# Optimization experiments

Hardware: AMD Instinct MI355X
Metric: run time of the kernel (lower is better)

Reference implementation:

```python
import jax, jax.numpy as jnp
import numpy as np

B, T, HID = 2, 2048, 1024
NH = 8
QK_DIM = 1024
V_DIM = 2048
SCALE_BASE = 512.0
GN_EPS = 1e-5


def _xpos_rotate(x, downscale):
    # x: [B, T, QK_DIM]; XPOS rotary embedding (syncdoth/RetNet, offset=0)
    d = QK_DIM
    dh = d // 2
    pos = jnp.arange(T, dtype=jnp.float32)
    # per-pair magnitude scale
    base_scale = (jnp.arange(0, d, 2, dtype=jnp.float32) + 0.4 * d) / (1.4 * d)  # [dh]
    scale = base_scale[None, :] ** (pos[:, None] / SCALE_BASE)  # [T, dh]
    if downscale:
        scale = 1.0 / scale
    inv_freq = 1.0 / (10000.0 ** (jnp.arange(dh, dtype=jnp.float32) / dh))
    sinusoid = pos[:, None] * inv_freq[None, :]  # [T, dh]
    sin = jnp.sin(sinusoid) * scale
    cos = jnp.cos(sinusoid) * scale
    # duplicate_interleave -> [T, d]
    sin = jnp.repeat(sin, 2, axis=-1)
    cos = jnp.repeat(cos, 2, axis=-1)
    x1 = x[..., 0::2]
    x2 = x[..., 1::2]
    rot = jnp.stack((-x2, x1), axis=-1).reshape(x.shape)  # rotate_every_two
    return x * cos[None] + rot * sin[None]


def setup_inputs() -> dict:
    key = jax.random.key(0)
    k1, k2, k3, k4 = jax.random.split(key, 4)
    x = jax.random.normal(k1, (B, T, HID), dtype=jnp.float32)
    Wqkv = jax.random.normal(k2, (HID, 2 * QK_DIM + V_DIM), dtype=jnp.float32) / np.sqrt(HID)
    Wg = jax.random.normal(k3, (HID, V_DIM), dtype=jnp.float32) / np.sqrt(HID)
    Wp = jax.random.normal(k4, (V_DIM, HID), dtype=jnp.float32) / np.sqrt(V_DIM)
    bp = jnp.zeros((HID,), dtype=jnp.float32)
    return {"x": x, "Wqkv": Wqkv, "Wg": Wg, "Wp": Wp, "bp": bp}


def reference(x, Wqkv, Wg, Wp, bp):
    # multi-scale decay (non-default gamma path)
    gamma = 1.0 - jnp.exp(jnp.linspace(np.log(1.0 / 32), np.log(1.0 / 512), NH)).astype(jnp.float32)  # [NH]

    qkv = x @ Wqkv  # [B,T,2qk+v]
    q, k, v = jnp.split(qkv, [QK_DIM, 2 * QK_DIM], axis=-1)
    q = _xpos_rotate(q, downscale=False)
    k = _xpos_rotate(k, downscale=True)

    dqk = QK_DIM // NH
    dv = V_DIM // NH
    q = q.reshape(B, T, NH, dqk).transpose(0, 2, 1, 3)  # [B,H,T,dqk]
    k = k.reshape(B, T, NH, dqk).transpose(0, 2, 1, 3)
    v = v.reshape(B, T, NH, dv).transpose(0, 2, 1, 3)   # [B,H,T,dv]

    # parallel decay mask: gamma^(i-j) for i>=j else 0  -> [H,T,T]
    idx = jnp.arange(T)
    expo = idx[:, None] - idx[None, :]
    expo_safe = jnp.where(expo >= 0, expo, 0).astype(jnp.float32)
    decay_mask = jnp.where(expo[None] >= 0, gamma[:, None, None] ** expo_safe[None], 0.0)  # [H,T,T]

    scores = jnp.einsum('bhid,bhjd->bhij', q, k) * (dqk ** -0.5)
    retention = jnp.einsum('bhij,bhjv->bhiv', scores * decay_mask[None], v)  # [B,H,T,dv]

    # current_kv state: sum_t decay_mask[h,-1,t] * k_t (outer) v_t  -> [B,H,dqk,dv]
    curr_kv = jnp.einsum('bhtk,bhtv,ht->bhkv', k, v, decay_mask[:, -1, :])

    ret = retention.transpose(0, 2, 1, 3).reshape(B, T, V_DIM)

    # GroupNorm(num_groups=NH, affine=False) over [B*T, V_DIM]
    g = ret.reshape(B, T, NH, dv)
    mu = jnp.mean(g, axis=-1, keepdims=True)
    var = jnp.var(g, axis=-1, keepdims=True)
    normed = ((g - mu) / jnp.sqrt(var + GN_EPS)).reshape(B, T, V_DIM)

    gate = jax.nn.silu(x @ Wg)
    out = (gate * normed) @ Wp + bp
    return out, curr_kv
```

## Files before the change

kernel.cpp:

```cpp
#include <hip/hip_runtime.h>

typedef unsigned short u16;
typedef unsigned int   u32;
typedef unsigned long long u64;

typedef __attribute__((ext_vector_type(8))) short bf8_t;
typedef __attribute__((ext_vector_type(4))) float f4_t;

#define DEVI __device__ __forceinline__
#define MFMA16(a,b,c) __builtin_amdgcn_mfma_f32_16x16x32_bf16((a),(b),(c),0,0,0)

#define BB   2
#define TT   2048
#define HIDN 1024
#define L0f  (-3.4657359027997265f)
#define DLf  (-0.3960841031714215f)
#define SCL  (0.08838834764831845f)

DEVI u16 f2b(float f) {
    u32 u = __float_as_uint(f);
    u += 0x7FFFu + ((u >> 16) & 1u);
    return (u16)(u >> 16);
}
DEVI float b2f(u16 u) { return __uint_as_float(((u32)u) << 16); }

DEVI void gll16(const void* g, void* l) {
    __builtin_amdgcn_global_load_lds((const __attribute__((address_space(1))) void*)g,
                                     (__attribute__((address_space(3))) void*)l, 16, 0, 0);
}

__global__ __launch_bounds__(256) void k_tables(u32* __restrict__ cqp, u32* __restrict__ ckp,
                                                float* __restrict__ gt, float* __restrict__ gk) {
    int bx = blockIdx.x;
    if (bx >= 4096) {
        int i = (bx - 4096) * 256 + threadIdx.x;
        if (i < 16384) {
            int h = i >> 11, t = i & 2047;
            float lg2 = log2f(1.f - expf(L0f + (float)h * DLf));
            gt[i] = exp2f((float)(2047 - t) * lg2);
        } else {
            int idx = i - 16384;
            int h = idx >> 6, d = idx & 63;
            float lg2 = log2f(1.f - expf(L0f + (float)h * DLf));
            gk[idx] = exp2f(-(float)d * lg2);
        }
        return;
    }
    int idx = bx * 256 + threadIdx.x;
    int t = idx >> 9, m = idx & 511;
    float base = (2.f * (float)m + 409.6f) * (1.f / 1433.6f);
    float s = exp2f(log2f(base) * ((float)t * (1.f / 512.f)));
    float invf = exp2f(-(float)m * (13.287712379549449f / 512.f));
    float sn, cs;
    sincosf((float)t * invf, &sn, &cs);
    int h = m >> 6;
    float lg2h = log2f(1.f - expf(L0f + (float)h * DLf));
    float qf = s * SCL * exp2f((float)(t & 63) * lg2h);
    cqp[idx] = (u32)f2b(cs * qf) | ((u32)f2b(sn * qf) << 16);
    float is = 1.f / s;
    ckp[idx] = (u32)f2b(cs * is) | ((u32)f2b(sn * is) << 16);
}

__global__ __launch_bounds__(256) void k_cvt(const float* __restrict__ in, u16* __restrict__ out) {
    int i = blockIdx.x * 256 + threadIdx.x;
    float4 v = ((const float4*)in)[i];
    u64 pk = (u64)f2b(v.x) | ((u64)f2b(v.y) << 16) | ((u64)f2b(v.z) << 32) | ((u64)f2b(v.w) << 48);
    ((u64*)out)[i] = pk;
}

__global__ __launch_bounds__(256) void k_tposeF(const float* __restrict__ Wqkv,
                                                const float* __restrict__ Wg,
                                                const float* __restrict__ Wp,
                                                u16* __restrict__ oQ, u16* __restrict__ oG,
                                                u16* __restrict__ oP) {
    __shared__ float tile[32][33];
    int bx = blockIdx.x;
    const float* in; u16* out; int R, C, cx, ry;
    if (bx < 4096)      { in = Wqkv; out = oQ; R = 1024; C = 4096; cx = bx & 127;        ry = bx >> 7; }
    else if (bx < 6144) { int b2 = bx - 4096; in = Wg; out = oG; R = 1024; C = 2048; cx = b2 & 63; ry = b2 >> 6; }
    else                { int b2 = bx - 6144; in = Wp; out = oP; R = 2048; C = 1024; cx = b2 & 31; ry = b2 >> 5; }
    int c0 = cx * 32, r0 = ry * 32;
    int tx = threadIdx.x, ty = threadIdx.y;
#pragma unroll
    for (int i = 0; i < 4; i++)
        tile[ty * 4 + i][tx] = in[(size_t)(r0 + ty * 4 + i) * C + c0 + tx];
    __syncthreads();
#pragma unroll
    for (int i = 0; i < 4; i++)
        out[(size_t)(c0 + ty * 4 + i) * R + r0 + tx] = f2b(tile[tx][ty * 4 + i]);
}

DEVI void stage_chunk(const u16* __restrict__ A, const u16* __restrict__ B,
                      int m0, int n0, int kt, char* buf, int id, int wid, int lane) {
    int j = id & 3;
    int flat = j * 8192 + wid * 1024 + lane * 16;
    int row = flat >> 7, byt = (flat & 127) ^ ((row & 7) << 4);
    if (id < 4)
        gll16((const char*)A + (size_t)(m0 + row) * 2048 + kt * 128 + byt,
              buf + j * 8192 + wid * 1024);
    else
        gll16((const char*)B + (size_t)(n0 + row) * 2048 + kt * 128 + byt,
              buf + 32768 + j * 8192 + wid * 1024);
}

#define QCORE(kk, fmh, LOADB)                                                         \
    {                                                                                 \
        bf8_t a_[4];                                                                  \
        _Pragma("unroll")                                                             \
        for (int f = 0; f < 4; f++) {                                                 \
            int ra = 128 * wr + ((fmh) * 4 + f) * 16 + lr;                            \
            a_[f] = *(const bf8_t*)(bA + ra * 128 + (((kk) * 64 + lg * 16) ^ ((ra & 7) << 4))); \
        }                                                                             \
        if (LOADB) {                                                                  \
            _Pragma("unroll")                                                         \
            for (int f = 0; f < 4; f++) {                                             \
                int rb = 64 * wc + f * 16 + lr;                                       \
                breg[f] = *(const bf8_t*)(bB + rb * 128 + (((kk) * 64 + lg * 16) ^ ((rb & 7) << 4))); \
            }                                                                         \
        }                                                                             \
        __builtin_amdgcn_s_barrier();                                                 \
        __builtin_amdgcn_s_setprio(1);                                                \
        _Pragma("unroll")                                                             \
        for (int f = 0; f < 4; f++)                                                   \
            _Pragma("unroll")                                                         \
            for (int j = 0; j < 4; j++)                                               \
                acc[(fmh) * 4 + f][j] = MFMA16(a_[f], breg[j], acc[(fmh) * 4 + f][j]); \
        __builtin_amdgcn_s_setprio(0);                                                \
    }

__global__ __launch_bounds__(512, 2) void k_gemm_qkvg8(
    const u16* __restrict__ xb, const u16* __restrict__ Wcat,
    const u32* __restrict__ cqp, const u32* __restrict__ ckp, const float* __restrict__ gkt,
    u16* __restrict__ qw, u16* __restrict__ kw, u16* __restrict__ kT, u16* __restrict__ vT,
    u16* __restrict__ gateb) {
    __shared__ __align__(16) char L[131072];
    int flat = blockIdx.x;
    int swz = (flat & 7) * 48 + (flat >> 3);
    int m0 = (swz / 24) * 256, n0 = (swz % 24) * 256;
    int tid = threadIdx.x, lane = tid & 63, wid = tid >> 6;
    int wr = wid >> 2, wc = wid & 3, lr = lane & 15, lg = lane >> 4;
    f4_t acc[8][4];
#pragma unroll
    for (int i = 0; i < 8; i++)
#pragma unroll
        for (int j = 0; j < 4; j++)
#pragma unroll
            for (int e = 0; e < 4; e++) acc[i][j][e] = 0.f;
    stage_chunk(xb, Wcat, m0, n0, 0, L, 0, wid, lane);
    stage_chunk(xb, Wcat, m0, n0, 0, L, 2, wid, lane);
    stage_chunk(xb, Wcat, m0, n0, 0, L, 4, wid, lane);
    stage_chunk(xb, Wcat, m0, n0, 0, L, 5, wid, lane);
    stage_chunk(xb, Wcat, m0, n0, 0, L, 6, wid, lane);
    stage_chunk(xb, Wcat, m0, n0, 0, L, 7, wid, lane);
    stage_chunk(xb, Wcat, m0, n0, 0, L, 1, wid, lane);
    stage_chunk(xb, Wcat, m0, n0, 0, L, 3, wid, lane);
    asm volatile("s_waitcnt vmcnt(2)" ::: "memory");
    __builtin_amdgcn_s_barrier();
    for (int kt = 0; kt < 16; ++kt) {
        const char* bA = L + (kt & 1) * 65536;
        const char* bB = bA + 32768;
        char* nbuf = L + ((kt + 1) & 1) * 65536;
        bf8_t breg[4];
        if (kt < 15) {
            stage_chunk(xb, Wcat, m0, n0, kt + 1, nbuf, 0, wid, lane);
            stage_chunk(xb, Wcat, m0, n0, kt + 1, nbuf, 2, wid, lane);
        }
        QCORE(0, 0, 1)
        if (kt < 15) { asm volatile("s_waitcnt vmcnt(2)" ::: "memory"); }
        else         { asm volatile("s_waitcnt vmcnt(0)" ::: "memory"); }
        __builtin_amdgcn_s_barrier();
        if (kt < 15) {
            stage_chunk(xb, Wcat, m0, n0, kt + 1, nbuf, 4, wid, lane);
            stage_chunk(xb, Wcat, m0, n0, kt + 1, nbuf, 5, wid, lane);
        }
        QCORE(0, 1, 0)
        __builtin_amdgcn_s_barrier();
        if (kt < 15) {
            stage_chunk(xb, Wcat, m0, n0, kt + 1, nbuf, 6, wid, lane);
            stage_chunk(xb, Wcat, m0, n0, kt + 1, nbuf, 7, wid, lane);
        }
        QCORE(1, 0, 1)
        __builtin_amdgcn_s_barrier();
        if (kt < 15) {
            stage_chunk(xb, Wcat, m0, n0, kt + 1, nbuf, 1, wid, lane);
            stage_chunk(xb, Wcat, m0, n0, kt + 1, nbuf, 3, wid, lane);
        }
        QCORE(1, 1, 0)
        if (kt < 15) { asm volatile("s_waitcnt vmcnt(2)" ::: "memory"); }
        __builtin_amdgcn_s_barrier();
    }
    __syncthreads();
    char* SP = L;
    int b = m0 >> 11, t0 = m0 & 2047;
    if (n0 < 4096 && n0 >= 2048) {
        int h = (n0 - 2048) >> 8;
#pragma unroll
        for (int fm = 0; fm < 8; fm++)
#pragma unroll
            for (int fn = 0; fn < 4; fn++) {
                int dv = wc * 64 + fn * 16 + lr;
                int rowb = wr * 128 + fm * 16 + lg * 4;
                u64 pk = 0;
#pragma unroll
                for (int r = 0; r < 4; r++) pk |= ((u64)f2b(acc[fm][fn][r])) << (16 * r);
                *(u64*)(SP + dv * 512 + ((rowb * 2) ^ ((dv & 15) << 4))) = pk;
            }
        __syncthreads();
#pragma unroll
        for (int it = 0; it < 16; it++) {
            int chunk = it * 512 + tid;
            int dv = chunk >> 5, j = chunk & 31;
            uint4 v = *(const uint4*)(SP + dv * 512 + ((j * 16) ^ ((dv & 15) << 4)));
            *(uint4*)(vT + ((size_t)((b * 8 + h) * 256 + dv)) * 2048 + t0 + j * 8) = v;
        }
    } else if (n0 < 2048) {
        int isK = n0 >= 1024;
        const u32* cT = isK ? ckp : cqp;
        int hb = (n0 >> 7) & 7;
#pragma unroll
        for (int fm = 0; fm < 8; fm++)
#pragma unroll
            for (int fn = 0; fn < 4; fn++) {
                int col = wc * 64 + fn * 16 + lr;
                int gq = (n0 & 1023) + col;
                int mi = gq >> 1, h = gq >> 7;
                u64 pk = 0;
#pragma unroll
                for (int r = 0; r < 4; r++) {
                    int rowl = wr * 128 + fm * 16 + lg * 4 + r;
                    int t = t0 + rowl;
                    float v = acc[fm][fn][r];
                    float pv = __shfl_xor(v, 1);
                    u32 cp = cT[t * 512 + mi];
                    float cs = b2f((u16)cp), sn = b2f((u16)(cp >> 16));
                    float o = (col & 1) ? (v * cs + pv * sn) : (v * cs - pv * sn);
                    if (isK) {
                        pk |= ((u64)f2b(o)) << (16 * r);
                        o *= gkt[h * 64 + (t & 63)];
                    }
                    *(u16*)(SP + rowl * 512 + ((col * 2) ^ ((rowl & 15) << 4))) = f2b(o);
                }
                if (isK)
                    *(u64*)&kT[((size_t)((b * 8 + h) * 128 + (gq & 127))) * 2048 + t0 + wr * 128 + fm * 16 + lg * 4] = pk;
            }
        __syncthreads();
#pragma unroll
        for (int it = 0; it < 16; it++) {
            int chunk = it * 512 + tid;
            int r = chunk >> 5, j = chunk & 31;
            uint4 v = *(const uint4*)(SP + r * 512 + ((j * 16) ^ ((r & 15) << 4)));
            int hh = hb + (j >> 4);
            u16* g = (isK ? kw : qw) + ((size_t)((b * 8 + hh) * 2048 + t0 + r)) * 128 + (j & 15) * 8;
            *(uint4*)g = v;
        }
    } else {
        int c0 = n0 - 4096;
#pragma unroll
        for (int fm = 0; fm < 8; fm++)
#pragma unroll
            for (int fn = 0; fn < 4; fn++) {
                int col = wc * 64 + fn * 16 + lr;
#pragma unroll
                for (int r = 0; r < 4; r++) {
                    int rowl = wr * 128 + fm * 16 + lg * 4 + r;
                    float gg = acc[fm][fn][r];
                    *(u16*)(SP + rowl * 512 + ((col * 2) ^ ((rowl & 15) << 4))) = f2b(gg / (1.f + expf(-gg)));
                }
            }
        __syncthreads();
#pragma unroll
        for (int it = 0; it < 16; it++) {
            int chunk = it * 512 + tid;
            int r = chunk >> 5, j = chunk & 31;
            uint4 v = *(const uint4*)(SP + r * 512 + ((j * 16) ^ ((r & 15) << 4)));
            *(uint4*)(gateb + (size_t)(b * 2048 + t0 + r) * 2048 + c0 + j * 8) = v;
        }
    }
}

DEVI void gemm_ml(const u16* __restrict__ Ag, const u16* __restrict__ Bg, int Klen, int Kstr,
                  int m0, int n0, u16* As, u16* Bs, f4_t acc[4][4]) {
    int tid = threadIdx.x, lane = tid & 63, wid = tid >> 6;
    int wr = wid >> 1, wc = wid & 1, lr = lane & 15, lg = lane >> 4;
    for (int k0 = 0; k0 < Klen; k0 += 64) {
        __syncthreads();
#pragma unroll
        for (int p = 0; p < 4; p++) {
            int flat = p * 4096 + tid * 16;
            int row = flat >> 7, byt = (flat & 127) ^ ((row & 7) << 4);
            gll16((const char*)Ag + ((size_t)(m0 + row) * Kstr + k0) * 2 + byt,
                  (char*)As + p * 4096 + wid * 1024);
            gll16((const char*)Bg + ((size_t)(n0 + row) * Kstr + k0) * 2 + byt,
                  (char*)Bs + p * 4096 + wid * 1024);
        }
        __syncthreads();
#pragma unroll
        for (int kk = 0; kk < 2; kk++) {
            bf8_t a[4], b[4];
#pragma unroll
            for (int f = 0; f < 4; f++) {
                int ra = wr * 64 + f * 16 + lr;
                a[f] = *(const bf8_t*)((const char*)As + ra * 128 + ((kk * 64 + lg * 16) ^ ((ra & 7) << 4)));
                int rb = wc * 64 + f * 16 + lr;
                b[f] = *(const bf8_t*)((const char*)Bs + rb * 128 + ((kk * 64 + lg * 16) ^ ((rb & 7) << 4)));
            }
#pragma unroll
            for (int i = 0; i < 4; i++)
#pragma unroll
                for (int j = 0; j < 4; j++)
                    acc[i][j] = MFMA16(a[i], b[j], acc[i][j]);
        }
    }
}

DEVI void acc_zero(f4_t acc[4][4]) {
#pragma unroll
    for (int i = 0; i < 4; i++)
#pragma unroll
        for (int j = 0; j < 4; j++)
#pragma unroll
            for (int e = 0; e < 4; e++) acc[i][j][e] = 0.f;
}

__global__ __launch_bounds__(256) void k_gemm_outp(const u16* __restrict__ gdb, const u16* __restrict__ Wt,
                                                   float* __restrict__ part) {
    __shared__ u16 SM[128 * 128];
    f4_t acc[4][4]; acc_zero(acc);
    int m0 = blockIdx.y * 128, n0 = blockIdx.x * 128, kz = blockIdx.z;
    gemm_ml(gdb + kz * 1024, Wt + kz * 1024, 1024, 2048, m0, n0, SM, SM + 128 * 64, acc);
    int tid = threadIdx.x, lane = tid & 63, wid = tid >> 6;
    int wr = wid >> 1, wc = wid & 1, lr = lane & 15, lg = lane >> 4;
    float* SMf = (float*)SM;
    float* po = part + (size_t)kz * 4096 * 1024;
    __syncthreads();
#pragma unroll
    for (int p = 0; p < 2; p++) {
        if (p) __syncthreads();
        if (wr == p) {
#pragma unroll
            for (int fm = 0; fm < 4; fm++)
#pragma unroll
                for (int fn = 0; fn < 4; fn++) {
                    int col = wc * 64 + fn * 16 + lr;
#pragma unroll
                    for (int r = 0; r < 4; r++) {
                        int rowl = fm * 16 + lg * 4 + r;
                        *(float*)((char*)SMf + rowl * 512 + ((col * 4) ^ ((rowl & 7) << 6))) = acc[fm][fn][r];
                    }
                }
        }
        __syncthreads();
#pragma unroll
        for (int it2 = 0; it2 < 8; it2++) {
            int chunk = it2 * 256 + tid;
            int rowl = chunk >> 5, j = chunk & 31;
            f4_t v = *(const f4_t*)((const char*)SMf + rowl * 512 + ((j * 16) ^ ((rowl & 7) << 6)));
            *(f4_t*)((char*)po + ((size_t)(m0 + p * 64 + rowl) * 1024 + n0) * 4 + j * 16) = v;
        }
    }
}

__global__ __launch_bounds__(256) void k_outred(const float* __restrict__ part, const float* __restrict__ bp,
                                                float* __restrict__ outp) {
    int i = blockIdx.x * 256 + threadIdx.x;
    f4_t a = ((const f4_t*)part)[i];
    f4_t c = ((const f4_t*)(part + (size_t)4096 * 1024))[i];
    f4_t bb = *(const f4_t*)(bp + ((i * 4) & 1023));
#pragma unroll
    for (int e = 0; e < 4; e++) a[e] += c[e] + bb[e];
    ((f4_t*)outp)[i] = a;
}

__global__ __launch_bounds__(256, 3) void k_retention(const u16* __restrict__ qws, const u16* __restrict__ kws,
                                                      const u16* __restrict__ vTws,
                                                      u16* __restrict__ ret0, u16* __restrict__ ret1) {
    __shared__ u16 SMr[64 * 128 + 256 * 64];
    u16* Ks = SMr;
    u16* Vs = SMr + 64 * 128;
    int x = blockIdx.x;
    int it, jlo, jhi, toret1;
    if (x < 16)      { it = 15 - x;  jlo = 0;              jhi = it + 1;         toret1 = 0; }
    else if (x < 32) { it = x;       jlo = 0;              jhi = (it + 2) >> 1;  toret1 = 0; }
    else             { it = x - 16;  jlo = (it + 2) >> 1;  jhi = it + 1;         toret1 = 1; }
    int h = blockIdx.y, b = blockIdx.z;
    int bh = b * 8 + h;
    float lg2 = log2f(1.f - expf(L0f + (float)h * DLf));
    int i0 = it * 64;
    const u16* qbase = qws + (size_t)bh * 2048 * 128;
    const u16* kbase = kws + (size_t)bh * 2048 * 128;
    const u16* vbase = vTws + (size_t)bh * 256 * 2048;
    int tid = threadIdx.x, lane = tid & 63, w = tid >> 6, lr = lane & 15, lg = lane >> 4;
    bf8_t aq[4];
#pragma unroll
    for (int kk = 0; kk < 4; kk++)
        aq[kk] = *(const bf8_t*)((const char*)qbase + (size_t)(i0 + w * 16 + lr) * 256 + kk * 64 + lg * 16);
    f4_t racc[16];
#pragma unroll
    for (int f = 0; f < 16; f++)
#pragma unroll
        for (int e = 0; e < 4; e++) racc[f][e] = 0.f;
    for (int jt = jlo; jt < jhi; jt++) {
        int j0 = jt * 64;
        int diag = (jt == it);
        float tf = exp2f(64.f * (float)(it - jt) * lg2);
        __syncthreads();
#pragma unroll
        for (int p = 0; p < 4; p++) {
            int flat = p * 4096 + tid * 16;
            int row = flat >> 8, byt = (flat & 255) ^ ((row & 7) << 4);
            gll16((const char*)kbase + (size_t)(j0 + row) * 256 + byt, (char*)Ks + p * 4096 + w * 1024);
        }
#pragma unroll
        for (int p = 0; p < 8; p++) {
            int flat = p * 4096 + tid * 16;
            int row = flat >> 7, byt = (flat & 127) ^ ((row & 7) << 4);
            gll16((const char*)vbase + (size_t)row * 4096 + (size_t)j0 * 2 + byt,
                  (char*)Vs + p * 4096 + w * 1024);
        }
        __syncthreads();
        f4_t sacc[4];
#pragma unroll
        for (int f = 0; f < 4; f++)
#pragma unroll
            for (int e = 0; e < 4; e++) sacc[f][e] = 0.f;
#pragma unroll
        for (int kk = 0; kk < 4; kk++)
#pragma unroll
            for (int fn = 0; fn < 4; fn++) {
                int rb = fn * 16 + lr;
                bf8_t bb = *(const bf8_t*)((const char*)Ks + rb * 256 + ((kk * 64 + lg * 16) ^ ((rb & 7) << 4)));
                sacc[fn] = MFMA16(aq[kk], bb, sacc[fn]);
            }
        __syncthreads();
#pragma unroll
        for (int fn = 0; fn < 4; fn++)
#pragma unroll
            for (int r = 0; r < 4; r++) {
                int i_loc = w * 16 + lg * 4 + r;
                int col = fn * 16 + lr;
                float v = diag ? ((i_loc - col >= 0) ? sacc[fn][r] : 0.f) : sacc[fn][r] * tf;
                *(u16*)((char*)Ks + i_loc * 128 + ((col * 2) ^ ((i_loc & 7) << 4))) = f2b(v);
            }
#pragma unroll
        for (int kk = 0; kk < 2; kk++) {
            int ra = w * 16 + lr;
            bf8_t ap = *(const bf8_t*)((const char*)Ks + ra * 128 + ((kk * 64 + lg * 16) ^ ((ra & 7) << 4)));
#pragma unroll
            for (int fn2 = 0; fn2 < 16; fn2++) {
                int rb = fn2 * 16 + lr;
                bf8_t bv = *(const bf8_t*)((const char*)Vs + rb * 128 + ((kk * 64 + lg * 16) ^ ((rb & 7) << 4)));
                racc[fn2] = MFMA16(ap, bv, racc[fn2]);
            }
        }
    }
    __syncthreads();
    u16* St = Vs;
#pragma unroll
    for (int fn2 = 0; fn2 < 16; fn2++)
#pragma unroll
        for (int r = 0; r < 4; r++) {
            int il = w * 16 + lg * 4 + r;
            int dv = fn2 * 16 + lr;
            *(u16*)((char*)St + il * 512 + ((dv * 2) ^ ((il & 15) << 4))) = f2b(racc[fn2][r]);
        }
    __syncthreads();
#pragma unroll
    for (int it2 = 0; it2 < 8; it2++) {
        int chunk = it2 * 256 + tid;
        int il = chunk >> 5, j = chunk & 31;
        uint4 v = *(const uint4*)((const char*)St + il * 512 + ((j * 16) ^ ((il & 15) << 4)));
        char* dst;
        if (toret1) dst = (char*)ret1 + ((size_t)(b * 1024 + i0 - 1024 + il) * 2048 + h * 256) * 2 + j * 16;
        else        dst = (char*)ret0 + ((size_t)(b * 2048 + i0 + il) * 2048 + h * 256) * 2 + j * 16;
        *(uint4*)dst = v;
    }
}

__global__ __launch_bounds__(512) void k_currkv(const u16* __restrict__ kTws, const u16* __restrict__ vTws,
                                                const float* __restrict__ gtab, float* __restrict__ part) {
    __shared__ u16 Ks2[128 * 64];
    __shared__ u16 Vws[256 * 64];
    int tr = blockIdx.x;
    int bh = blockIdx.y;
    int h = bh & 7;
    const u16* kT = kTws + (size_t)bh * 128 * 2048;
    const u16* vT = vTws + (size_t)bh * 256 * 2048;
    const float* gt = gtab + h * 2048;
    int tid = threadIdx.x, lane = tid & 63, wid = tid >> 6;
    int wr = wid >> 2, wc = wid & 3, lr = lane & 15, lg = lane >> 4;
    f4_t acc[4][4]; acc_zero(acc);
    for (int tc = 0; tc < 8; tc++) {
        int t0 = tr * 512 + tc * 64;
        __syncthreads();
#pragma unroll
        for (int p = 0; p < 2; p++) {
            int flat = p * 8192 + tid * 16;
            int row = flat >> 7, byt = (flat & 127) ^ ((row & 7) << 4);
            gll16((const char*)kT + (size_t)row * 4096 + (size_t)t0 * 2 + byt,
                  (char*)Ks2 + p * 8192 + wid * 1024);
        }
#pragma unroll
        for (int p = 0; p < 4; p++) {
            int flat = p * 8192 + tid * 16;
            int row = flat >> 7, byt = flat & 127;
            int tt = t0 + (byt >> 1);
            const u16* src = vT + (size_t)row * 2048 + tt;
            u16 tmp[8]; *(uint4*)tmp = *(const uint4*)src;
            const float* gp = gt + tt;
            u16 op[8];
#pragma unroll
            for (int e = 0; e < 8; e++) op[e] = f2b(b2f(tmp[e]) * gp[e]);
            *(uint4*)((char*)Vws + row * 128 + (byt ^ ((row & 7) << 4))) = *(uint4*)op;
        }
        __syncthreads();
#pragma unroll
        for (int kk = 0; kk < 2; kk++) {
            bf8_t a[4], bb[4];
#pragma unroll
            for (int f = 0; f < 4; f++) {
                int ra = wr * 64 + f * 16 + lr;
                a[f] = *(const bf8_t*)((const char*)Ks2 + ra * 128 + ((kk * 64 + lg * 16) ^ ((ra & 7) << 4)));
                int rb = wc * 64 + f * 16 + lr;
                bb[f] = *(const bf8_t*)((const char*)Vws + rb * 128 + ((kk * 64 + lg * 16) ^ ((rb & 7) << 4)));
            }
#pragma unroll
            for (int i = 0; i < 4; i++)
#pragma unroll
                for (int j = 0; j < 4; j++)
                    acc[i][j] = MFMA16(a[i], bb[j], acc[i][j]);
        }
    }
#pragma unroll
    for (int fm = 0; fm < 4; fm++)
#pragma unroll
        for (int fn = 0; fn < 4; fn++)
#pragma unroll
            for (int r = 0; r < 4; r++) {
                int dk = wr * 64 + fm * 16 + lg * 4 + r;
                int dv = wc * 64 + fn * 16 + lr;
                part[((size_t)(bh * 4 + tr)) * 32768 + (size_t)dk * 256 + dv] = acc[fm][fn][r];
            }
}

__global__ __launch_bounds__(256) void k_reduce_ckv(const float* __restrict__ part, float* __restrict__ outc) {
    int i = blockIdx.x * 256 + threadIdx.x;
    int bh = i >> 15, wv = i & 32767;
    float s = 0.f;
#pragma unroll
    for (int tr = 0; tr < 4; tr++) s += part[((size_t)(bh * 4 + tr)) * 32768 + wv];
    outc[i] = s;
}

__global__ __launch_bounds__(256) void k_gnorm(const u16* __restrict__ ret0, const u16* __restrict__ ret1,
                                               const u16* __restrict__ gateb, u16* __restrict__ gatedb) {
    int g = blockIdx.x * 4 + (threadIdx.x >> 6);
    int lane = threadIdx.x & 63;
    int row = g >> 3, h = g & 7;
    size_t base = (size_t)row * 2048 + h * 256 + lane * 4;
    u64 p0 = *(const u64*)(ret0 + base);
    float e0 = b2f((u16)p0), e1 = b2f((u16)(p0 >> 16)), e2 = b2f((u16)(p0 >> 32)), e3 = b2f((u16)(p0 >> 48));
    if ((row & 2047) >= 1024) {
        size_t b1 = (size_t)((row >> 11) * 1024 + (row & 1023)) * 2048 + h * 256 + lane * 4;
        u64 p1 = *(const u64*)(ret1 + b1);
        e0 += b2f((u16)p1); e1 += b2f((u16)(p1 >> 16)); e2 += b2f((u16)(p1 >> 32)); e3 += b2f((u16)(p1 >> 48));
    }
    float s = e0 + e1 + e2 + e3;
    float sqs = e0 * e0 + e1 * e1 + e2 * e2 + e3 * e3;
#pragma unroll
    for (int m = 1; m < 64; m <<= 1) { s += __shfl_xor(s, m); sqs += __shfl_xor(sqs, m); }
    float mean = s * (1.f / 256.f);
    float var = sqs * (1.f / 256.f) - mean * mean;
    float inv = rsqrtf(var + 1e-5f);
    u64 gp = *(const u64*)(gateb + base);
    u64 pk = (u64)f2b((e0 - mean) * inv * b2f((u16)gp)) |
             ((u64)f2b((e1 - mean) * inv * b2f((u16)(gp >> 16))) << 16) |
             ((u64)f2b((e2 - mean) * inv * b2f((u16)(gp >> 32))) << 32) |
             ((u64)f2b((e3 - mean) * inv * b2f((u16)(gp >> 48))) << 48);
    *(u64*)(gatedb + base) = pk;
}

extern "C" void kernel_launch(void* const* d_in, const int* in_sizes, int n_in,
                              void* d_out, int out_size, void* d_ws, size_t ws_size,
                              hipStream_t stream) {
    const float* x    = (const float*)d_in[0];
    const float* Wqkv = (const float*)d_in[1];
    const float* Wg   = (const float*)d_in[2];
    const float* Wp   = (const float*)d_in[3];
    const float* bp   = (const float*)d_in[4];
    float* outp   = (float*)d_out;
    float* outckv = outp + (size_t)BB * TT * HIDN;

    char* ws = (char*)d_ws;
    const size_t MB = 1024 * 1024;
    u16*   xb     = (u16*)(ws);
    u16*   WqkvT  = (u16*)(ws + 8 * MB);
    u16*   WgT    = (u16*)(ws + 16 * MB);
    u16*   WpT    = (u16*)(ws + 20 * MB);
    u32*   cqp    = (u32*)(ws + 24 * MB);
    u32*   ckp    = (u32*)(ws + 28 * MB);
    u16*   gateb  = (u16*)(ws + 32 * MB);
    u16*   qw     = (u16*)(ws + 48 * MB);
    u16*   kw     = (u16*)(ws + 56 * MB);
    u16*   kT     = (u16*)(ws + 64 * MB);
    u16*   vT     = (u16*)(ws + 72 * MB);
    u16*   ret0b  = (u16*)(ws + 88 * MB);
    u16*   ret1b  = (u16*)(ws + 104 * MB);
    float* ckvp   = (float*)(ws + 112 * MB);
    float* gtab   = (float*)(ws + 120 * MB);
    float* gkt    = (float*)(ws + 120 * MB + 65536);
    u16*   gatedb = (u16*)(ws + 48 * MB);
    float* opart  = (float*)(ws + 88 * MB);

    hipLaunchKernelGGL(k_tables, dim3(4162), dim3(256), 0, stream, cqp, ckp, gtab, gkt);
    hipLaunchKernelGGL(k_cvt, dim3(4096), dim3(256), 0, stream, x, xb);
    hipLaunchKernelGGL(k_tposeF, dim3(8192), dim3(32, 8), 0, stream, Wqkv, Wg, Wp, WqkvT, WgT, WpT);
    hipLaunchKernelGGL(k_gemm_qkvg8, dim3(384), dim3(512), 0, stream,
                       xb, WqkvT, cqp, ckp, gkt, qw, kw, kT, vT, gateb);
    hipLaunchKernelGGL(k_currkv, dim3(4, 16), dim3(512), 0, stream, kT, vT, gtab, ckvp);
    hipLaunchKernelGGL(k_reduce_ckv, dim3(2048), dim3(256), 0, stream, ckvp, outckv);
    hipLaunchKernelGGL(k_retention, dim3(48, 8, 2), dim3(256), 0, stream, qw, kw, vT, ret0b, ret1b);
    hipLaunchKernelGGL(k_gnorm, dim3(8192), dim3(256), 0, stream, ret0b, ret1b, gateb, gatedb);
    hipLaunchKernelGGL(k_gemm_outp, dim3(8, 32, 2), dim3(256), 0, stream, gatedb, WpT, opart);
    hipLaunchKernelGGL(k_outred, dim3(4096), dim3(256), 0, stream, opart, bp, outp);
}
```

Before: 225.8 us.

## Replace split-K output GEMM with double-buffered full-K kernel fusing bias

Replaces the split-K output projection GEMM and its separate reduction kernel with one kernel. Each 128x128 tile now runs the full K=2048 using 8 waves, double-buffered LDS staging with prefetch of the next k-tile, and raised wave priority around the MFMAs. Bias is added in the epilogue, which removes the 32 MB partial write and read-back and one kernel launch. The grid shrinks from 512 to 256 blocks, which may lower occupancy and latency hiding.

```diff
diff --git a/kernel.cpp b/kernel.cpp
--- a/kernel.cpp
+++ b/kernel.cpp
@@ -278,38 +278,97 @@
     }
 }
 
-DEVI void gemm_ml(const u16* __restrict__ Ag, const u16* __restrict__ Bg, int Klen, int Kstr,
-                  int m0, int n0, u16* As, u16* Bs, f4_t acc[4][4]) {
+DEVI void stage_o(const u16* __restrict__ A, const u16* __restrict__ B,
+                  int m0, int n0, int kt, char* buf, int id, int wid, int lane) {
+    int j = id & 1;
+    int flat = j * 8192 + wid * 1024 + lane * 16;
+    int row = flat >> 7, byt = (flat & 127) ^ ((row & 7) << 4);
+    if (id < 2)
+        gll16((const char*)A + (size_t)(m0 + row) * 4096 + kt * 128 + byt,
+              buf + j * 8192 + wid * 1024);
+    else
+        gll16((const char*)B + (size_t)(n0 + row) * 4096 + kt * 128 + byt,
+              buf + 16384 + j * 8192 + wid * 1024);
+}
+
+__global__ __launch_bounds__(512, 2) void k_gemm_out2(const u16* __restrict__ gdb,
+                                                      const u16* __restrict__ Wt,
+                                                      const float* __restrict__ bp,
+                                                      float* __restrict__ outp) {
+    __shared__ __align__(16) char Lo[65536];
+    int m0 = blockIdx.y * 128, n0 = blockIdx.x * 128;
     int tid = threadIdx.x, lane = tid & 63, wid = tid >> 6;
     int wr = wid >> 1, wc = wid & 1, lr = lane & 15, lg = lane >> 4;
-    for (int k0 = 0; k0 < Klen; k0 += 64) {
-        __syncthreads();
-#pragma unroll
-        for (int p = 0; p < 4; p++) {
-            int flat = p * 4096 + tid * 16;
-            int row = flat >> 7, byt = (flat & 127) ^ ((row & 7) << 4);
-            gll16((const char*)Ag + ((size_t)(m0 + row) * Kstr + k0) * 2 + byt,
-                  (char*)As + p * 4096 + wid * 1024);
-            gll16((const char*)Bg + ((size_t)(n0 + row) * Kstr + k0) * 2 + byt,
-                  (char*)Bs + p * 4096 + wid * 1024);
-        }
-        __syncthreads();
+    f4_t acc[2][4];
+#pragma unroll
+    for (int i = 0; i < 2; i++)
+#pragma unroll
+        for (int j = 0; j < 4; j++)
+#pragma unroll
+            for (int e = 0; e < 4; e++) acc[i][j][e] = 0.f;
+    stage_o(gdb, Wt, m0, n0, 0, Lo, 0, wid, lane);
+    stage_o(gdb, Wt, m0, n0, 0, Lo, 1, wid, lane);
+    stage_o(gdb, Wt, m0, n0, 0, Lo, 2, wid, lane);
+    stage_o(gdb, Wt, m0, n0, 0, Lo, 3, wid, lane);
+    asm volatile("s_waitcnt vmcnt(0)" ::: "memory");
+    __builtin_amdgcn_s_barrier();
+    for (int kt = 0; kt < 32; ++kt) {
+        const char* bA = Lo + (kt & 1) * 32768;
+        const char* bB = bA + 16384;
+        char* nbuf = Lo + ((kt + 1) & 1) * 32768;
+        if (kt < 31) {
+            stage_o(gdb, Wt, m0, n0, kt + 1, nbuf, 0, wid, lane);
+            stage_o(gdb, Wt, m0, n0, kt + 1, nbuf, 1, wid, lane);
+            stage_o(gdb, Wt, m0, n0, kt + 1, nbuf, 2, wid, lane);
+            stage_o(gdb, Wt, m0, n0, kt + 1, nbuf, 3, wid, lane);
+        }
+        __builtin_amdgcn_s_setprio(1);
 #pragma unroll
         for (int kk = 0; kk < 2; kk++) {
-            bf8_t a[4], b[4];
+            bf8_t a[2], b[4];
+#pragma unroll
+            for (int f = 0; f < 2; f++) {
+                int ra = wr * 32 + f * 16 + lr;
+                a[f] = *(const bf8_t*)(bA + ra * 128 + ((kk * 64 + lg * 16) ^ ((ra & 7) << 4)));
+            }
 #pragma unroll
             for (int f = 0; f < 4; f++) {
-                int ra = wr * 64 + f * 16 + lr;
-                a[f] = *(const bf8_t*)((const char*)As + ra * 128 + ((kk * 64 + lg * 16) ^ ((ra & 7) << 4)));
                 int rb = wc * 64 + f * 16 + lr;
-                b[f] = *(const bf8_t*)((const char*)Bs + rb * 128 + ((kk * 64 + lg * 16) ^ ((rb & 7) << 4)));
-            }
-#pragma unroll
-            for (int i = 0; i < 4; i++)
+                b[f] = *(const bf8_t*)(bB + rb * 128 + ((kk * 64 + lg * 16) ^ ((rb & 7) << 4)));
+            }
+#pragma unroll
+            for (int i = 0; i < 2; i++)
 #pragma unroll
                 for (int j = 0; j < 4; j++)
                     acc[i][j] = MFMA16(a[i], b[j], acc[i][j]);
         }
+        __builtin_amdgcn_s_setprio(0);
+        asm volatile("s_waitcnt vmcnt(0)" ::: "memory");
+        __builtin_amdgcn_s_barrier();
+    }
+    __syncthreads();
+    float* SMf = (float*)Lo;
+    float bv[4];
+#pragma unroll
+    for (int fn = 0; fn < 4; fn++) bv[fn] = bp[n0 + wc * 64 + fn * 16 + lr];
+#pragma unroll
+    for (int fm = 0; fm < 2; fm++)
+#pragma unroll
+        for (int fn = 0; fn < 4; fn++) {
+            int col = wc * 64 + fn * 16 + lr;
+#pragma unroll
+            for (int r = 0; r < 4; r++) {
+                int rowl = wr * 32 + fm * 16 + lg * 4 + r;
+                *(float*)((char*)SMf + rowl * 512 + ((col * 4) ^ ((rowl & 7) << 6))) = acc[fm][fn][r] + bv[fn];
+            }
+        }
+    __syncthreads();
+#pragma unroll
+    for (int it2 = 0; it2 < 8; it2++) {
+        int chunk = it2 * 512 + tid;
+        int rowl = chunk >> 5, j = chunk & 31;
+        f4_t v = *(const f4_t*)((const char*)SMf + rowl * 512 + ((j * 16) ^ ((rowl & 7) << 6)));
+        *(f4_t*)((char*)outp + ((size_t)(m0 + rowl) * 1024 + n0) * 4 + j * 16) = v;
     }
 }
 
@@ -320,55 +379,6 @@
         for (int j = 0; j < 4; j++)
 #pragma unroll
             for (int e = 0; e < 4; e++) acc[i][j][e] = 0.f;
-}
-
-__global__ __launch_bounds__(256) void k_gemm_outp(const u16* __restrict__ gdb, const u16* __restrict__ Wt,
-                                                   float* __restrict__ part) {
-    __shared__ u16 SM[128 * 128];
-    f4_t acc[4][4]; acc_zero(acc);
-    int m0 = blockIdx.y * 128, n0 = blockIdx.x * 128, kz = blockIdx.z;
-    gemm_ml(gdb + kz * 1024, Wt + kz * 1024, 1024, 2048, m0, n0, SM, SM + 128 * 64, acc);
-    int tid = threadIdx.x, lane = tid & 63, wid = tid >> 6;
-    int wr = wid >> 1, wc = wid & 1, lr = lane & 15, lg = lane >> 4;
-    float* SMf = (float*)SM;
-    float* po = part + (size_t)kz * 4096 * 1024;
-    __syncthreads();
-#pragma unroll
-    for (int p = 0; p < 2; p++) {
-        if (p) __syncthreads();
-        if (wr == p) {
-#pragma unroll
-            for (int fm = 0; fm < 4; fm++)
-#pragma unroll
-                for (int fn = 0; fn < 4; fn++) {
-                    int col = wc * 64 + fn * 16 + lr;
-#pragma unroll
-                    for (int r = 0; r < 4; r++) {
-                        int rowl = fm * 16 + lg * 4 + r;
-                        *(float*)((char*)SMf + rowl * 512 + ((col * 4) ^ ((rowl & 7) << 6))) = acc[fm][fn][r];
-                    }
-                }
-        }
-        __syncthreads();
-#pragma unroll
-        for (int it2 = 0; it2 < 8; it2++) {
-            int chunk = it2 * 256 + tid;
-            int rowl = chunk >> 5, j = chunk & 31;
-            f4_t v = *(const f4_t*)((const char*)SMf + rowl * 512 + ((j * 16) ^ ((rowl & 7) << 6)));
-            *(f4_t*)((char*)po + ((size_t)(m0 + p * 64 + rowl) * 1024 + n0) * 4 + j * 16) = v;
-        }
-    }
-}
-
-__global__ __launch_bounds__(256) void k_outred(const float* __restrict__ part, const float* __restrict__ bp,
-                                                float* __restrict__ outp) {
-    int i = blockIdx.x * 256 + threadIdx.x;
-    f4_t a = ((const f4_t*)part)[i];
-    f4_t c = ((const f4_t*)(part + (size_t)4096 * 1024))[i];
-    f4_t bb = *(const f4_t*)(bp + ((i * 4) & 1023));
-#pragma unroll
-    for (int e = 0; e < 4; e++) a[e] += c[e] + bb[e];
-    ((f4_t*)outp)[i] = a;
 }
 
 __global__ __launch_bounds__(256, 3) void k_retention(const u16* __restrict__ qws, const u16* __restrict__ kws,
@@ -609,7 +619,6 @@
     float* gtab   = (float*)(ws + 120 * MB);
     float* gkt    = (float*)(ws + 120 * MB + 65536);
     u16*   gatedb = (u16*)(ws + 48 * MB);
-    float* opart  = (float*)(ws + 88 * MB);
 
     hipLaunchKernelGGL(k_tables, dim3(4162), dim3(256), 0, stream, cqp, ckp, gtab, gkt);
     hipLaunchKernelGGL(k_cvt, dim3(4096), dim3(256), 0, stream, x, xb);
@@ -620,6 +629,5 @@
     hipLaunchKernelGGL(k_reduce_ckv, dim3(2048), dim3(256), 0, stream, ckvp, outckv);
     hipLaunchKernelGGL(k_retention, dim3(48, 8, 2), dim3(256), 0, stream, qw, kw, vT, ret0b, ret1b);
     hipLaunchKernelGGL(k_gnorm, dim3(8192), dim3(256), 0, stream, ret0b, ret1b, gateb, gatedb);
-    hipLaunchKernelGGL(k_gemm_outp, dim3(8, 32, 2), dim3(256), 0, stream, gatedb, WpT, opart);
-    hipLaunchKernelGGL(k_outred, dim3(4096), dim3(256), 0, stream, opart, bp, outp);
-}
+    hipLaunchKernelGGL(k_gemm_out2, dim3(8, 32), dim3(512), 0, stream, gatedb, WpT, bp, outp);
+}
```

After: 216.7 us. 1.04x faster.
